# Performance work log

Measured on AMD Instinct MI355X. Metric: run time of the kernel, lower is better.

Reference implementation:

```python
import jax, jax.numpy as jnp
import numpy as np

def setup_inputs() -> dict:
    key = jax.random.key(0)
    k1, k2, k3 = jax.random.split(key, 3)
    shape = (2, 2048, 8, 64)  # [n, l, h, d]
    return {
        "q": jax.random.normal(k1, shape, dtype=jnp.float32),
        "k": jax.random.normal(k2, shape, dtype=jnp.float32),
        "v": jax.random.normal(k3, shape, dtype=jnp.float32),
    }

def reference(q, k, v):
    # QK^T: [n, l, s, h]
    qk = jnp.einsum('nlhd,nshd->nlsh', q, k)
    softmax_temp = 1.0 / (q.shape[3] ** 0.5)
    attn = jax.nn.softmax(softmax_temp * qk, axis=2)
    # weighted values: [n, l, h, d]
    return jnp.einsum('nlsh,nshd->nlhd', attn, v)
```

## Files before the change

kernel.cpp:

```cpp
#include <hip/hip_runtime.h>
#include <hip/hip_bf16.h>
#include <math.h>

typedef float floatx16 __attribute__((ext_vector_type(16)));
typedef __bf16 bf16x8 __attribute__((ext_vector_type(8)));

#define SEQ 2048
#define NH 8
#define DH 64
#define NB 2
#define HEADS 16
#define HSTRIDE (SEQ * DH)
#define TILE_E (64 * 64)

__device__ __forceinline__ unsigned short f2bf(float x) {
  union { __bf16 b; unsigned short u; } c; c.b = (__bf16)x; return c.u;
}
__device__ __forceinline__ unsigned int pk2bf(float a, float b) {
  union { __hip_bfloat162 h2; unsigned int u; } c;
  c.h2 = __float22bfloat162_rn(make_float2(a, b));
  return c.u;
}

__global__ __launch_bounds__(256)
void pack_kv(const float* __restrict__ k, const float* __restrict__ v,
             unsigned short* __restrict__ kb, unsigned short* __restrict__ vb) {
  __shared__ unsigned short Ts[64][68];
  const int tid  = threadIdx.x;
  const int bx   = blockIdx.x;
  const int kt   = bx & 31;
  const int head = bx >> 5;
  const int n = head >> 3, h = head & 7;

  #pragma unroll
  for (int j2 = 0; j2 < 2; ++j2) {
    int c = j2 * 256 + tid;
    int lane = c & 63;
    int kk = (c >> 6) & 3, ks2 = c >> 8;
    int row = kt * 64 + ks2 * 32 + (lane & 31);
    int d0  = kk * 16 + (lane >> 5) * 8;
    const float* src = k + ((size_t)(n * SEQ + row) * NH + h) * DH + d0;
    float4 a = *(const float4*)src;
    float4 b = *(const float4*)(src + 4);
    ushort4 lo, hi;
    lo.x = f2bf(a.x); lo.y = f2bf(a.y); lo.z = f2bf(a.z); lo.w = f2bf(a.w);
    hi.x = f2bf(b.x); hi.y = f2bf(b.y); hi.z = f2bf(b.z); hi.w = f2bf(b.w);
    unsigned short* dst = kb + (size_t)head * HSTRIDE + kt * TILE_E + c * 8;
    *(ushort4*)dst = lo;
    *(ushort4*)(dst + 4) = hi;
  }

  #pragma unroll
  for (int i = 0; i < 4; ++i) {
    int id = i * 256 + tid;
    int s  = id >> 4;
    int c4 = (id & 15) * 4;
    size_t g = ((size_t)((n * SEQ + kt * 64 + s) * NH + h)) * DH + c4;
    float4 x = *(const float4*)(v + g);
    ushort4 y;
    y.x = f2bf(x.x); y.y = f2bf(x.y); y.z = f2bf(x.z); y.w = f2bf(x.w);
    *(ushort4*)&Ts[s][c4] = y;
  }
  __syncthreads();
  #pragma unroll
  for (int j2 = 0; j2 < 2; ++j2) {
    int c = j2 * 256 + tid;
    int lane = c & 63;
    int dsub = (c >> 6) & 1, ss = c >> 7;
    int s0 = ss * 16 + (lane >> 5) * 8;
    int d  = dsub * 32 + (lane & 31);
    ushort4 lo, hi;
    lo.x = Ts[s0 + 0][d]; lo.y = Ts[s0 + 1][d]; lo.z = Ts[s0 + 2][d]; lo.w = Ts[s0 + 3][d];
    hi.x = Ts[s0 + 4][d]; hi.y = Ts[s0 + 5][d]; hi.z = Ts[s0 + 6][d]; hi.w = Ts[s0 + 7][d];
    unsigned short* dst = vb + (size_t)head * HSTRIDE + kt * TILE_E + c * 8;
    *(ushort4*)dst = lo;
    *(ushort4*)(dst + 4) = hi;
  }
}

__device__ __forceinline__ void halfswap(unsigned a, unsigned b, bool lo,
                                         unsigned& outA, unsigned& outB) {
  unsigned m = lo ? b : a;
  unsigned sx = (unsigned)__shfl_xor((int)m, 32, 64);
  outA = lo ? a : sx;
  outB = lo ? sx : b;
}

#define SMEM_BYTES 35328

__global__ __launch_bounds__(512)
void attn(const float* __restrict__ q, const unsigned short* __restrict__ kb,
          const unsigned short* __restrict__ vt, float* __restrict__ out) {
  __shared__ __align__(16) char smem[SMEM_BYTES];
  float* oM = (float*)smem;
  float* lM = (float*)(smem + 8 * 16 * 68 * 4);

  const int tid  = threadIdx.x;
  const int wave = tid >> 6;
  const int lane = tid & 63;
  const int l32  = lane & 31;
  const int hl   = lane >> 5;
  const bool lo  = (hl == 0);

  const int bx   = blockIdx.x;
  const int head = bx & 15;
  const int qg   = bx >> 4;
  const int n = head >> 3, h = head & 7;

  const unsigned short* kf = kb + (size_t)head * HSTRIDE;
  const unsigned short* vf = vt + (size_t)head * HSTRIDE;

  bf16x8 qB[2][4];
  #pragma unroll
  for (int qs = 0; qs < 2; ++qs)
    #pragma unroll
    for (int kk = 0; kk < 4; ++kk) {
      const int row = qg * 64 + qs * 32 + l32;
      const float* src = q + ((size_t)((n * SEQ + row) * NH + h)) * DH + kk * 16 + hl * 8;
      float4 x0 = *(const float4*)src;
      float4 x1 = *(const float4*)(src + 4);
      union { unsigned int u32[4]; bf16x8 v8; } u;
      u.u32[0] = pk2bf(x0.x, x0.y); u.u32[1] = pk2bf(x0.z, x0.w);
      u.u32[2] = pk2bf(x1.x, x1.y); u.u32[3] = pk2bf(x1.z, x1.w);
      qB[qs][kk] = u.v8;
    }

  floatx16 o[2][2];
  float lsum[2];
  #pragma unroll
  for (int qs = 0; qs < 2; ++qs) {
    lsum[qs] = 0.f;
    #pragma unroll
    for (int d = 0; d < 2; ++d)
      #pragma unroll
      for (int i = 0; i < 16; ++i) o[qs][d][i] = 0.f;
  }

  const float S = 0.125f * 1.4426950408889634f;
  const float C = 12.0f;

  for (int it = 0; it < 4; ++it) {
    const int kt = it * 8 + wave;
    const unsigned short* kt_base = kf + kt * TILE_E;
    const unsigned short* vt_base = vf + kt * TILE_E;

    #pragma unroll
    for (int ks2 = 0; ks2 < 2; ++ks2) {
      bf16x8 kA[4];
      #pragma unroll
      for (int kk = 0; kk < 4; ++kk)
        kA[kk] = *(const bf16x8*)(kt_base + ((ks2 * 4 + kk) * 64 + lane) * 8);
      bf16x8 vB[2][2];
      #pragma unroll
      for (int ssl = 0; ssl < 2; ++ssl)
        #pragma unroll
        for (int dsub = 0; dsub < 2; ++dsub)
          vB[ssl][dsub] = *(const bf16x8*)(vt_base + (((ks2 * 2 + ssl) * 2 + dsub) * 64 + lane) * 8);

      #pragma unroll
      for (int qs = 0; qs < 2; ++qs) {
        floatx16 acc;
        #pragma unroll
        for (int i = 0; i < 16; ++i) acc[i] = 0.f;
        #pragma unroll
        for (int kk = 0; kk < 4; ++kk)
          acc = __builtin_amdgcn_mfma_f32_32x32x16_bf16(kA[kk], qB[qs][kk], acc, 0, 0, 0);

        unsigned pk[8];
        #pragma unroll
        for (int g2 = 0; g2 < 4; ++g2) {
          float p0 = __builtin_amdgcn_exp2f(acc[4 * g2 + 0] * S - C);
          float p1 = __builtin_amdgcn_exp2f(acc[4 * g2 + 1] * S - C);
          float p2 = __builtin_amdgcn_exp2f(acc[4 * g2 + 2] * S - C);
          float p3 = __builtin_amdgcn_exp2f(acc[4 * g2 + 3] * S - C);
          lsum[qs] += (p0 + p1) + (p2 + p3);
          pk[g2 * 2]     = pk2bf(p0, p1);
          pk[g2 * 2 + 1] = pk2bf(p2, p3);
        }

        union { unsigned u32[4]; bf16x8 v8; } A1, A2;
        halfswap(pk[0], pk[2], lo, A1.u32[0], A1.u32[2]);
        halfswap(pk[1], pk[3], lo, A1.u32[1], A1.u32[3]);
        halfswap(pk[4], pk[6], lo, A2.u32[0], A2.u32[2]);
        halfswap(pk[5], pk[7], lo, A2.u32[1], A2.u32[3]);

        o[qs][0] = __builtin_amdgcn_mfma_f32_32x32x16_bf16(A1.v8, vB[0][0], o[qs][0], 0, 0, 0);
        o[qs][1] = __builtin_amdgcn_mfma_f32_32x32x16_bf16(A1.v8, vB[0][1], o[qs][1], 0, 0, 0);
        o[qs][0] = __builtin_amdgcn_mfma_f32_32x32x16_bf16(A2.v8, vB[1][0], o[qs][0], 0, 0, 0);
        o[qs][1] = __builtin_amdgcn_mfma_f32_32x32x16_bf16(A2.v8, vB[1][1], o[qs][1], 0, 0, 0);
      }
    }
  }

  #pragma unroll
  for (int qs = 0; qs < 2; ++qs)
    lsum[qs] += __shfl_xor(lsum[qs], 32, 64);

  const int mrow = tid >> 5;
  const int mcol = (tid & 31) * 2;
  #pragma unroll
  for (int p = 0; p < 4; ++p) {
    const int qsub = p >> 1, rh = p & 1;
    __syncthreads();
    #pragma unroll
    for (int r8 = 0; r8 < 8; ++r8) {
      const int r   = rh * 8 + r8;
      const int rip = (r8 & 3) + 4 * hl + 8 * (r8 >> 2);
      oM[(wave * 16 + rip) * 68 + l32]      = o[qsub][0][r];
      oM[(wave * 16 + rip) * 68 + 32 + l32] = o[qsub][1][r];
    }
    if (lane < 32 && ((lane >> 4) & 1) == rh) lM[wave * 16 + (lane & 15)] = lsum[qsub];
    __syncthreads();
    float v0 = 0.f, v1 = 0.f, l = 0.f;
    #pragma unroll
    for (int w = 0; w < 8; ++w) {
      float2 t2 = *(const float2*)&oM[(w * 16 + mrow) * 68 + mcol];
      v0 += t2.x; v1 += t2.y;
      l += lM[w * 16 + mrow];
    }
    float inv = 1.f / l;
    const int grow = qg * 64 + p * 16 + mrow;
    float2 st; st.x = v0 * inv; st.y = v1 * inv;
    *(float2*)(out + ((size_t)((n * SEQ + grow) * NH + h)) * DH + mcol) = st;
  }
}

extern "C" void kernel_launch(void* const* d_in, const int* in_sizes, int n_in,
                              void* d_out, int out_size, void* d_ws, size_t ws_size,
                              hipStream_t stream) {
  const float* q = (const float*)d_in[0];
  const float* k = (const float*)d_in[1];
  const float* v = (const float*)d_in[2];
  float* out = (float*)d_out;
  (void)in_sizes; (void)n_in; (void)out_size; (void)ws_size;

  unsigned short* kb = (unsigned short*)d_ws;
  unsigned short* vb = kb + (size_t)HEADS * HSTRIDE;

  pack_kv<<<HEADS * (SEQ / 64), 256, 0, stream>>>(k, v, kb, vb);
  attn<<<HEADS * (SEQ / 64), 512, 0, stream>>>(q, kb, vb, out);
}
```

Measured before the change: 107.1 us.

## Use permlane32 swap, hoist K/V loads, interleave QK MFMA with softmax

Replaces the shuffle-based half-wave swap (ds_bpermute via __shfl_xor plus selects) with v_permlane32_swap_b32 inline asm. A runtime probe detects the operand semantics and picks the forward or reversed form. All K and V fragments for a tile are now loaded up front, and the second query block's QK MFMAs are issued between the first block's exp/pack and its PV MFMAs. This is meant to overlap matrix and VALU work and to cut cross-lane traffic, at the cost of higher register pressure at 512 threads per block.

Measured after the change: 105.9 us. About the same (-1.1%).

```diff
diff --git a/kernel.cpp b/kernel.cpp
--- a/kernel.cpp
+++ b/kernel.cpp
@@ -20,6 +20,13 @@
   union { __hip_bfloat162 h2; unsigned int u; } c;
   c.h2 = __float22bfloat162_rn(make_float2(a, b));
   return c.u;
+}
+
+__device__ __forceinline__ void hswap_fwd(unsigned& a, unsigned& b) {
+  asm volatile("v_permlane32_swap_b32 %0, %1" : "+v"(a), "+v"(b));
+}
+__device__ __forceinline__ void hswap_rev(unsigned& a, unsigned& b) {
+  asm volatile("v_permlane32_swap_b32 %0, %1" : "+v"(b), "+v"(a));
 }
 
 __global__ __launch_bounds__(256)
@@ -78,14 +85,6 @@
   }
 }
 
-__device__ __forceinline__ void halfswap(unsigned a, unsigned b, bool lo,
-                                         unsigned& outA, unsigned& outB) {
-  unsigned m = lo ? b : a;
-  unsigned sx = (unsigned)__shfl_xor((int)m, 32, 64);
-  outA = lo ? a : sx;
-  outB = lo ? sx : b;
-}
-
 #define SMEM_BYTES 35328
 
 __global__ __launch_bounds__(512)
@@ -100,7 +99,10 @@
   const int lane = tid & 63;
   const int l32  = lane & 31;
   const int hl   = lane >> 5;
-  const bool lo  = (hl == 0);
+
+  unsigned px = (unsigned)lane, py = (unsigned)lane + 100u;
+  hswap_fwd(px, py);
+  const bool mir = (__builtin_amdgcn_readfirstlane(px) != 0u);
 
   const int bx   = blockIdx.x;
   const int head = bx & 15;
@@ -144,50 +146,67 @@
     const unsigned short* kt_base = kf + kt * TILE_E;
     const unsigned short* vt_base = vf + kt * TILE_E;
 
+    bf16x8 kA[2][4];
+    #pragma unroll
+    for (int ks2 = 0; ks2 < 2; ++ks2)
+      #pragma unroll
+      for (int kk = 0; kk < 4; ++kk)
+        kA[ks2][kk] = *(const bf16x8*)(kt_base + ((ks2 * 4 + kk) * 64 + lane) * 8);
+    bf16x8 vB[4][2];
+    #pragma unroll
+    for (int ss = 0; ss < 4; ++ss)
+      #pragma unroll
+      for (int dsub = 0; dsub < 2; ++dsub)
+        vB[ss][dsub] = *(const bf16x8*)(vt_base + ((ss * 2 + dsub) * 64 + lane) * 8);
+
     #pragma unroll
     for (int ks2 = 0; ks2 < 2; ++ks2) {
-      bf16x8 kA[4];
+      floatx16 acc2[2];
+      #pragma unroll
+      for (int i = 0; i < 16; ++i) acc2[0][i] = 0.f;
       #pragma unroll
       for (int kk = 0; kk < 4; ++kk)
-        kA[kk] = *(const bf16x8*)(kt_base + ((ks2 * 4 + kk) * 64 + lane) * 8);
-      bf16x8 vB[2][2];
-      #pragma unroll
-      for (int ssl = 0; ssl < 2; ++ssl)
-        #pragma unroll
-        for (int dsub = 0; dsub < 2; ++dsub)
-          vB[ssl][dsub] = *(const bf16x8*)(vt_base + (((ks2 * 2 + ssl) * 2 + dsub) * 64 + lane) * 8);
-
-      #pragma unroll
-      for (int qs = 0; qs < 2; ++qs) {
-        floatx16 acc;
-        #pragma unroll
-        for (int i = 0; i < 16; ++i) acc[i] = 0.f;
-        #pragma unroll
-        for (int kk = 0; kk < 4; ++kk)
-          acc = __builtin_amdgcn_mfma_f32_32x32x16_bf16(kA[kk], qB[qs][kk], acc, 0, 0, 0);
-
+        acc2[0] = __builtin_amdgcn_mfma_f32_32x32x16_bf16(kA[ks2][kk], qB[0][kk], acc2[0], 0, 0, 0);
+
+      #pragma unroll
+      for (int m = 0; m < 2; ++m) {
         unsigned pk[8];
         #pragma unroll
         for (int g2 = 0; g2 < 4; ++g2) {
-          float p0 = __builtin_amdgcn_exp2f(acc[4 * g2 + 0] * S - C);
-          float p1 = __builtin_amdgcn_exp2f(acc[4 * g2 + 1] * S - C);
-          float p2 = __builtin_amdgcn_exp2f(acc[4 * g2 + 2] * S - C);
-          float p3 = __builtin_amdgcn_exp2f(acc[4 * g2 + 3] * S - C);
-          lsum[qs] += (p0 + p1) + (p2 + p3);
+          float p0 = __builtin_amdgcn_exp2f(acc2[m][4 * g2 + 0] * S - C);
+          float p1 = __builtin_amdgcn_exp2f(acc2[m][4 * g2 + 1] * S - C);
+          float p2 = __builtin_amdgcn_exp2f(acc2[m][4 * g2 + 2] * S - C);
+          float p3 = __builtin_amdgcn_exp2f(acc2[m][4 * g2 + 3] * S - C);
+          lsum[m] += (p0 + p1) + (p2 + p3);
           pk[g2 * 2]     = pk2bf(p0, p1);
           pk[g2 * 2 + 1] = pk2bf(p2, p3);
         }
 
+        if (m == 0) {
+          #pragma unroll
+          for (int i = 0; i < 16; ++i) acc2[1][i] = 0.f;
+          #pragma unroll
+          for (int kk = 0; kk < 4; ++kk)
+            acc2[1] = __builtin_amdgcn_mfma_f32_32x32x16_bf16(kA[ks2][kk], qB[1][kk], acc2[1], 0, 0, 0);
+        }
+
         union { unsigned u32[4]; bf16x8 v8; } A1, A2;
-        halfswap(pk[0], pk[2], lo, A1.u32[0], A1.u32[2]);
-        halfswap(pk[1], pk[3], lo, A1.u32[1], A1.u32[3]);
-        halfswap(pk[4], pk[6], lo, A2.u32[0], A2.u32[2]);
-        halfswap(pk[5], pk[7], lo, A2.u32[1], A2.u32[3]);
-
-        o[qs][0] = __builtin_amdgcn_mfma_f32_32x32x16_bf16(A1.v8, vB[0][0], o[qs][0], 0, 0, 0);
-        o[qs][1] = __builtin_amdgcn_mfma_f32_32x32x16_bf16(A1.v8, vB[0][1], o[qs][1], 0, 0, 0);
-        o[qs][0] = __builtin_amdgcn_mfma_f32_32x32x16_bf16(A2.v8, vB[1][0], o[qs][0], 0, 0, 0);
-        o[qs][1] = __builtin_amdgcn_mfma_f32_32x32x16_bf16(A2.v8, vB[1][1], o[qs][1], 0, 0, 0);
+        A1.u32[0] = pk[0]; A1.u32[2] = pk[2];
+        A1.u32[1] = pk[1]; A1.u32[3] = pk[3];
+        A2.u32[0] = pk[4]; A2.u32[2] = pk[6];
+        A2.u32[1] = pk[5]; A2.u32[3] = pk[7];
+        if (!mir) {
+          hswap_fwd(A1.u32[0], A1.u32[2]); hswap_fwd(A1.u32[1], A1.u32[3]);
+          hswap_fwd(A2.u32[0], A2.u32[2]); hswap_fwd(A2.u32[1], A2.u32[3]);
+        } else {
+          hswap_rev(A1.u32[0], A1.u32[2]); hswap_rev(A1.u32[1], A1.u32[3]);
+          hswap_rev(A2.u32[0], A2.u32[2]); hswap_rev(A2.u32[1], A2.u32[3]);
+        }
+
+        o[m][0] = __builtin_amdgcn_mfma_f32_32x32x16_bf16(A1.v8, vB[ks2 * 2][0],     o[m][0], 0, 0, 0);
+        o[m][1] = __builtin_amdgcn_mfma_f32_32x32x16_bf16(A1.v8, vB[ks2 * 2][1],     o[m][1], 0, 0, 0);
+        o[m][0] = __builtin_amdgcn_mfma_f32_32x32x16_bf16(A2.v8, vB[ks2 * 2 + 1][0], o[m][0], 0, 0, 0);
+        o[m][1] = __builtin_amdgcn_mfma_f32_32x32x16_bf16(A2.v8, vB[ks2 * 2 + 1][1], o[m][1], 0, 0, 0);
       }
     }
   }
```
